# Kernel optimization log

Hardware: AMD Instinct MI355X
Metric: run time of the kernel (lower is better)

The kernel has to match this reference:

```python
import jax, jax.numpy as jnp
import numpy as np

B, N, D = 2, 1024, 64
H, DK, DV = 4, 16, 16
DOUT = 128
STEPS = 3


def _ln(x, eps, w=None, b=None):
    mu = jnp.mean(x, axis=-1, keepdims=True)
    var = jnp.mean((x - mu) ** 2, axis=-1, keepdims=True)
    y = (x - mu) * jax.lax.rsqrt(var + eps)
    if w is not None:
        y = y * w + b
    return y


def setup_inputs() -> dict:
    key = jax.random.key(0)
    ks = jax.random.split(key, 16)
    q_x = jax.random.normal(ks[0], (B, N, D), jnp.float32)
    v_x = jax.random.normal(ks[1], (B, N, D), jnp.float32)
    qa = jax.random.uniform(ks[2], (B, N, N), jnp.float32)
    va = jax.random.uniform(ks[3], (B, N, N), jnp.float32)
    q_adj = qa / jnp.sum(qa, axis=-1, keepdims=True)  # row-normalized adjacency
    v_adj = va / jnp.sum(va, axis=-1, keepdims=True)
    s = 0.05
    w_qs = jax.random.normal(ks[4], (D, H * DK), jnp.float32) * s
    w_ks = jax.random.normal(ks[5], (D, H * DK), jnp.float32) * s
    w_vs = jax.random.normal(ks[6], (D, H * DV), jnp.float32) * s
    w_fc = jax.random.normal(ks[7], (H * DV, D), jnp.float32) * s
    mha_ln_w = jnp.ones((D,), jnp.float32)
    mha_ln_b = jnp.zeros((D,), jnp.float32)
    conv_w = jax.random.normal(ks[8], (D, DOUT), jnp.float32) * s
    conv_b = jnp.zeros((DOUT,), jnp.float32)
    lin_w = jax.random.normal(ks[9], (DOUT, D), jnp.float32) * s
    lin_b = jnp.zeros((D,), jnp.float32)
    norm_w = jnp.ones((D,), jnp.float32)
    norm_b = jnp.zeros((D,), jnp.float32)
    return dict(q_x=q_x, q_adj=q_adj, v_x=v_x, v_adj=v_adj,
                w_qs=w_qs, w_ks=w_ks, w_vs=w_vs, w_fc=w_fc,
                mha_ln_w=mha_ln_w, mha_ln_b=mha_ln_b,
                conv_w=conv_w, conv_b=conv_b, lin_w=lin_w, lin_b=lin_b,
                norm_w=norm_w, norm_b=norm_b)


def reference(q_x, q_adj, v_x, v_adj, w_qs, w_ks, w_vs, w_fc,
              mha_ln_w, mha_ln_b, conv_w, conv_b, lin_w, lin_b,
              norm_w, norm_b):
    b, n, d = q_x.shape
    residual = q_x
    qs, vs = [q_x], [v_x]
    q1 = jnp.einsum('bij,bjd->bid', q_adj, q_x)
    v1 = jnp.einsum('bij,bjd->bid', v_adj, v_x)
    qs.append(q1); vs.append(v1)
    for _ in range(2, STEPS):
        q1 = jnp.einsum('bij,bjd->bid', q_adj, q1)
        v1 = jnp.einsum('bij,bjd->bid', v_adj, v1)
        qs.append(q1); vs.append(v1)
    qc = _ln(jnp.concatenate(qs, axis=1), 1e-5)  # [b, STEPS*n, d]
    vc = _ln(jnp.concatenate(vs, axis=1), 1e-5)
    L = qc.shape[1]
    # multi-head attention (dropout = identity in eval)
    q = (qc @ w_qs).reshape(b, L, H, DK)
    k = (qc @ w_ks).reshape(b, L, H, DK)
    v = (vc @ w_vs).reshape(b, L, H, DV)
    scores = jnp.einsum('bqhd,bkhd->bhqk', q, k) / jnp.asarray(DK ** 0.5, q.dtype)
    attn = jax.nn.softmax(scores, axis=-1)
    o = jnp.einsum('bhqk,bkhd->bqhd', attn, v).reshape(b, L, H * DV)
    o = o @ w_fc + qc
    o = _ln(o, 1e-6, mha_ln_w, mha_ln_b)
    # pool across diffusion steps (faithful to original reshape semantics)
    x = jnp.mean(o.reshape(b, n, -1, STEPS), axis=-1)  # [b, n, d]
    x1 = jax.nn.relu(x @ conv_w + conv_b)
    x = residual + x1 @ lin_w + lin_b
    return _ln(x, 1e-5, norm_w, norm_b)
```

## Files before the change

kernel.cpp:

```cpp
#include <hip/hip_runtime.h>
#include <hip/hip_bf16.h>

#define B_ 2
#define N_ 1024
#define D_ 64
#define L_ 3072
#define H_ 4

typedef __attribute__((ext_vector_type(8))) short s8v;
typedef __attribute__((ext_vector_type(4))) short s4v;
typedef __attribute__((ext_vector_type(4))) float f32x4;

#define EXP2F(x) __builtin_amdgcn_exp2f(x)
#define QSCALE 0.36067376022224085f

__device__ __forceinline__ float wave_sum64(float v) {
#pragma unroll
    for (int off = 32; off > 0; off >>= 1) v += __shfl_xor(v, off, 64);
    return v;
}

__device__ __forceinline__ short f2bf(float f) {
    unsigned u = __float_as_uint(f);
    u += 0x7FFFu + ((u >> 16) & 1u);
    return (short)(u >> 16);
}
__device__ __forceinline__ unsigned cvt_pk_bf16(float a, float b) {
    unsigned r;
    asm("v_cvt_pk_bf16_f32 %0, %1, %2" : "=v"(r) : "v"(a), "v"(b));
    return r;
}
union pk8 { s8v v; unsigned u[4]; };
union pk4 { s4v v; unsigned u[2]; };

__device__ __forceinline__ s8v ldfrag_full(const __hip_bfloat16* p0, const __hip_bfloat16* p1) {
    s4v a = *reinterpret_cast<const s4v*>(p0);
    s4v b = *reinterpret_cast<const s4v*>(p1);
    s8v r;
    r[0] = a[0]; r[1] = a[1]; r[2] = a[2]; r[3] = a[3];
    r[4] = b[0]; r[5] = b[1]; r[6] = b[2]; r[7] = b[3];
    return r;
}
__device__ __forceinline__ s8v wfrag_build(const float* __restrict__ W, int N, int ct, int ks,
                                           int lo, int hi, float scale) {
    s8v r;
    int n = ct * 16 + lo;
    int k0 = ks * 32 + 4 * hi;
#pragma unroll
    for (int j = 0; j < 4; ++j) {
        r[j]     = f2bf(W[(k0 + j) * N + n] * scale);
        r[4 + j] = f2bf(W[(k0 + 16 + j) * N + n] * scale);
    }
    return r;
}

__global__ void xpose(const float* __restrict__ xq, const float* __restrict__ xv,
                      __hip_bfloat16* __restrict__ xtq, __hip_bfloat16* __restrict__ xtv) {
    __shared__ short ts[64][65];
    int m = blockIdx.y;
    int qv = m >> 1, b = m & 1;
    int l0 = blockIdx.x * 64;
    const float* x = (qv ? xv : xq) + (size_t)b * N_ * 64;
    int t = threadIdx.x;
#pragma unroll
    for (int i = 0; i < 4; ++i) {
        int f = t + i * 256;
        int r = f >> 4, c4 = f & 15;
        float4 v = *reinterpret_cast<const float4*>(x + (size_t)(l0 + r) * 64 + c4 * 4);
        ts[c4 * 4 + 0][r] = f2bf(v.x);
        ts[c4 * 4 + 1][r] = f2bf(v.y);
        ts[c4 * 4 + 2][r] = f2bf(v.z);
        ts[c4 * 4 + 3][r] = f2bf(v.w);
    }
    __syncthreads();
    short* xt = reinterpret_cast<short*>(qv ? xtv : xtq) + (size_t)b * 64 * N_;
#pragma unroll
    for (int i = 0; i < 4; ++i) {
        int f = t + i * 256;
        int d = f >> 4, seg = f & 15;
        s4v o;
        o[0] = ts[d][seg * 4 + 0]; o[1] = ts[d][seg * 4 + 1];
        o[2] = ts[d][seg * 4 + 2]; o[3] = ts[d][seg * 4 + 3];
        *reinterpret_cast<s4v*>(xt + (size_t)d * N_ + l0 + seg * 4) = o;
    }
}

__global__ __launch_bounds__(256) void spmm_mfma(
        const float* __restrict__ adj_q, const float* __restrict__ adj_v,
        const __hip_bfloat16* __restrict__ xtq, const __hip_bfloat16* __restrict__ xtv,
        float* __restrict__ oq, float* __restrict__ ov,
        __hip_bfloat16* __restrict__ oqt, __hip_bfloat16* __restrict__ ovt, int writet) {
    const int lane = threadIdx.x & 63;
    const int w = threadIdx.x >> 6;
    const int lo = lane & 15, hi = lane >> 4;
    const int rt = blockIdx.x;
    const int qv = blockIdx.y, b = blockIdx.z;

    const float* adj = (qv ? adj_v : adj_q) + (size_t)b * N_ * N_ + (size_t)(rt * 16 + lo) * N_;
    const __hip_bfloat16* xt = (qv ? xtv : xtq) + ((size_t)b * 64 + w * 16 + lo) * N_;

    f32x4 acc = {0.f, 0.f, 0.f, 0.f};
#pragma unroll 8
    for (int ks = 0; ks < 32; ++ks) {
        int k0 = ks * 32;
        float4 a4 = *reinterpret_cast<const float4*>(adj + k0 + 4 * hi);
        float4 b4 = *reinterpret_cast<const float4*>(adj + k0 + 16 + 4 * hi);
        pk8 af;
        af.u[0] = cvt_pk_bf16(a4.x, a4.y); af.u[1] = cvt_pk_bf16(a4.z, a4.w);
        af.u[2] = cvt_pk_bf16(b4.x, b4.y); af.u[3] = cvt_pk_bf16(b4.z, b4.w);
        s8v xf = ldfrag_full(xt + k0 + 4 * hi, xt + k0 + 16 + 4 * hi);
        acc = __builtin_amdgcn_mfma_f32_16x16x32_bf16(xf, af.v, acc, 0, 0, 0);
    }
    float* o = (qv ? ov : oq) + ((size_t)b * N_ + rt * 16 + lo) * 64 + w * 16 + 4 * hi;
    *reinterpret_cast<f32x4*>(o) = acc;
    if (writet) {
        short* ot = reinterpret_cast<short*>(qv ? ovt : oqt) + (size_t)b * 64 * N_;
#pragma unroll
        for (int j = 0; j < 4; ++j)
            ot[(size_t)(w * 16 + 4 * hi + j) * N_ + rt * 16 + lo] = f2bf(acc[j]);
    }
}

__global__ void concat_ln(const float* __restrict__ qx, const float* __restrict__ q1,
                          const float* __restrict__ q2,
                          const float* __restrict__ vx, const float* __restrict__ v1,
                          const float* __restrict__ v2,
                          float* __restrict__ qc,
                          __hip_bfloat16* __restrict__ qcb, __hip_bfloat16* __restrict__ vcb) {
    int rid  = blockIdx.x * 4 + (threadIdx.x >> 6);
    int lane = threadIdx.x & 63;
    int qvsel = rid >= (B_ * L_);
    int r = qvsel ? rid - B_ * L_ : rid;
    int b = r / L_, l = r % L_;
    int s = l / N_, i = l % N_;
    const float* src;
    if (!qvsel) src = (s == 0) ? qx : (s == 1) ? q1 : q2;
    else        src = (s == 0) ? vx : (s == 1) ? v1 : v2;
    float v = src[((size_t)b * N_ + i) * D_ + lane];
    float mean = wave_sum64(v) * (1.0f / 64.0f);
    float d = v - mean;
    float var = wave_sum64(d * d) * (1.0f / 64.0f);
    float y = d * rsqrtf(var + 1e-5f);
    size_t o = ((size_t)b * L_ + l) * D_ + lane;
    if (!qvsel) {
        qc[o] = y;
        reinterpret_cast<short*>(qcb)[o] = f2bf(y);
    } else {
        reinterpret_cast<short*>(vcb)[o] = f2bf(y);
    }
}

__global__ __launch_bounds__(256) void gemm_qkv(
        const __hip_bfloat16* __restrict__ qcb, const __hip_bfloat16* __restrict__ vcb,
        const float* __restrict__ wq, const float* __restrict__ wk, const float* __restrict__ wv,
        __hip_bfloat16* __restrict__ qpk, __hip_bfloat16* __restrict__ kpk,
        __hip_bfloat16* __restrict__ vpk) {
    const int w = threadIdx.x >> 6;
    const int lane = threadIdx.x & 63;
    const int lo = lane & 15, hi = lane >> 4;
    const int ct0 = w * 3;

    s8v wf[3][2];
#pragma unroll
    for (int c = 0; c < 3; ++c) {
        int ct = ct0 + c;
        const float* W = (ct < 4) ? wq : (ct < 8) ? wk : wv;
        float sc = (ct < 4) ? QSCALE : 1.0f;
        wf[c][0] = wfrag_build(W, 64, ct & 3, 0, lo, hi, sc);
        wf[c][1] = wfrag_build(W, 64, ct & 3, 1, lo, hi, sc);
    }
    const bool needq = (ct0 < 8);
    const bool needv = (ct0 + 2 >= 8);
    const f32x4 zz = {0.f, 0.f, 0.f, 0.f};

#pragma unroll
    for (int rr = 0; rr < 2; ++rr) {
        int rt = blockIdx.x * 2 + rr;
        int rbase = rt * 16;
        int b = rbase / L_;
        int lloc = rbase % L_;
        int t32 = lloc >> 5;
        int half = (lloc >> 4) & 1;
        s8v aq0, aq1, av0, av1;
        if (needq) {
            const __hip_bfloat16* ar = qcb + (size_t)(rbase + lo) * 64;
            aq0 = ldfrag_full(ar + 4 * hi, ar + 16 + 4 * hi);
            aq1 = ldfrag_full(ar + 32 + 4 * hi, ar + 48 + 4 * hi);
        }
        if (needv) {
            const __hip_bfloat16* ar = vcb + (size_t)(rbase + lo) * 64;
            av0 = ldfrag_full(ar + 4 * hi, ar + 16 + 4 * hi);
            av1 = ldfrag_full(ar + 32 + 4 * hi, ar + 48 + 4 * hi);
        }
#pragma unroll
        for (int c = 0; c < 3; ++c) {
            int ct = ct0 + c;
            f32x4 acc = zz;
            if (ct < 8) {
                acc = __builtin_amdgcn_mfma_f32_16x16x32_bf16(wf[c][0], aq0, acc, 0, 0, 0);
                acc = __builtin_amdgcn_mfma_f32_16x16x32_bf16(wf[c][1], aq1, acc, 0, 0, 0);
                int h = ct & 3;
                int bh = b * H_ + h;
                short* dst = reinterpret_cast<short*>((ct < 4) ? qpk : kpk);
                pk4 o;
                o.u[0] = cvt_pk_bf16(acc[0], acc[1]);
                o.u[1] = cvt_pk_bf16(acc[2], acc[3]);
                *reinterpret_cast<s4v*>(dst +
                    (((size_t)bh * 96 + t32) * 64 + lane) * 8 + half * 4) = o.v;
            } else {
                acc = __builtin_amdgcn_mfma_f32_16x16x32_bf16(wf[c][0], av0, acc, 0, 0, 0);
                acc = __builtin_amdgcn_mfma_f32_16x16x32_bf16(wf[c][1], av1, acc, 0, 0, 0);
                int h = ct - 8;
                int bh = b * H_ + h;
                short* vt = reinterpret_cast<short*>(vpk);
                size_t base = ((size_t)bh * 96 + t32) * 64 * 8;
#pragma unroll
                for (int j = 0; j < 4; ++j) {
                    int lanep = (lo >> 2) * 16 + (4 * hi + j);
                    vt[base + (size_t)lanep * 8 + half * 4 + (lo & 3)] = f2bf(acc[j]);
                }
            }
        }
    }
}

__global__ __launch_bounds__(512) void attn_mfma(
        const __hip_bfloat16* __restrict__ qpk, const __hip_bfloat16* __restrict__ kpk,
        const __hip_bfloat16* __restrict__ vpk, __hip_bfloat16* __restrict__ attnob) {
    const int lane = threadIdx.x & 63;
    const int kg = threadIdx.x >> 6;
    const int g = blockIdx.x;
    const int bh = g / 96;
    const int tp = g % 96;
    const int b = bh >> 2, h = bh & 3;
    const int lo = lane & 15, hi = lane >> 4;

    const s8v* kp = reinterpret_cast<const s8v*>(kpk) + ((size_t)bh * 96) * 64 + lane;
    const s8v* vp = reinterpret_cast<const s8v*>(vpk) + ((size_t)bh * 96) * 64 + lane;
    const s8v* qp = reinterpret_cast<const s8v*>(qpk) + ((size_t)bh * 96 + tp) * 64 + lane;

    s8v q8 = *qp;
    s8v qfA = {q8[0], q8[1], q8[2], q8[3], 0, 0, 0, 0};
    s8v qfB = {q8[4], q8[5], q8[6], q8[7], 0, 0, 0, 0};

    f32x4 accA = {0.f, 0.f, 0.f, 0.f}, accB = {0.f, 0.f, 0.f, 0.f};
    float lsA = 0.f, lsB = 0.f;
    const f32x4 zz = {0.f, 0.f, 0.f, 0.f};

    const int t0 = kg * 12;
    s8v kb0 = kp[(size_t)(t0 + 0) * 64];
    s8v vb0 = vp[(size_t)(t0 + 0) * 64];
    s8v kb1 = kp[(size_t)(t0 + 1) * 64];
    s8v vb1 = vp[(size_t)(t0 + 1) * 64];

#pragma unroll
    for (int i = 0; i < 12; ++i) {
        s8v ck, cv;
        if ((i & 1) == 0) { ck = kb0; cv = vb0; }
        else              { ck = kb1; cv = vb1; }
        int pf = (i + 2 < 12) ? t0 + i + 2 : t0;
        if ((i & 1) == 0) { kb0 = kp[(size_t)pf * 64]; vb0 = vp[(size_t)pf * 64]; }
        else              { kb1 = kp[(size_t)pf * 64]; vb1 = vp[(size_t)pf * 64]; }

        s8v kf0 = {ck[0], ck[1], ck[2], ck[3], 0, 0, 0, 0};
        s8v kf1 = {ck[4], ck[5], ck[6], ck[7], 0, 0, 0, 0};

        f32x4 s0A = __builtin_amdgcn_mfma_f32_16x16x32_bf16(kf0, qfA, zz, 0, 0, 0);
        f32x4 s1A = __builtin_amdgcn_mfma_f32_16x16x32_bf16(kf1, qfA, zz, 0, 0, 0);
        f32x4 s0B = __builtin_amdgcn_mfma_f32_16x16x32_bf16(kf0, qfB, zz, 0, 0, 0);
        f32x4 s1B = __builtin_amdgcn_mfma_f32_16x16x32_bf16(kf1, qfB, zz, 0, 0, 0);

        float pA0 = EXP2F(s0A[0]), pA1 = EXP2F(s0A[1]), pA2 = EXP2F(s0A[2]), pA3 = EXP2F(s0A[3]);
        float pA4 = EXP2F(s1A[0]), pA5 = EXP2F(s1A[1]), pA6 = EXP2F(s1A[2]), pA7 = EXP2F(s1A[3]);
        float pB0 = EXP2F(s0B[0]), pB1 = EXP2F(s0B[1]), pB2 = EXP2F(s0B[2]), pB3 = EXP2F(s0B[3]);
        float pB4 = EXP2F(s1B[0]), pB5 = EXP2F(s1B[1]), pB6 = EXP2F(s1B[2]), pB7 = EXP2F(s1B[3]);
        lsA += ((pA0 + pA1) + (pA2 + pA3)) + ((pA4 + pA5) + (pA6 + pA7));
        lsB += ((pB0 + pB1) + (pB2 + pB3)) + ((pB4 + pB5) + (pB6 + pB7));

        pk8 pfA, pfB;
        pfA.u[0] = cvt_pk_bf16(pA0, pA1); pfA.u[1] = cvt_pk_bf16(pA2, pA3);
        pfA.u[2] = cvt_pk_bf16(pA4, pA5); pfA.u[3] = cvt_pk_bf16(pA6, pA7);
        pfB.u[0] = cvt_pk_bf16(pB0, pB1); pfB.u[1] = cvt_pk_bf16(pB2, pB3);
        pfB.u[2] = cvt_pk_bf16(pB4, pB5); pfB.u[3] = cvt_pk_bf16(pB6, pB7);

        accA = __builtin_amdgcn_mfma_f32_16x16x32_bf16(cv, pfA.v, accA, 0, 0, 0);
        accB = __builtin_amdgcn_mfma_f32_16x16x32_bf16(cv, pfB.v, accB, 0, 0, 0);
    }

    lsA += __shfl_xor(lsA, 16, 64); lsA += __shfl_xor(lsA, 32, 64);
    lsB += __shfl_xor(lsB, 16, 64); lsB += __shfl_xor(lsB, 32, 64);

    __shared__ float red[8][2][64][5];
    red[kg][0][lane][0] = accA[0]; red[kg][0][lane][1] = accA[1];
    red[kg][0][lane][2] = accA[2]; red[kg][0][lane][3] = accA[3];
    red[kg][0][lane][4] = lsA;
    red[kg][1][lane][0] = accB[0]; red[kg][1][lane][1] = accB[1];
    red[kg][1][lane][2] = accB[2]; red[kg][1][lane][3] = accB[3];
    red[kg][1][lane][4] = lsB;
    __syncthreads();
    if (kg < 2) {
        int t = kg;
        float a0 = 0.f, a1 = 0.f, a2 = 0.f, a3 = 0.f, lt = 0.f;
#pragma unroll
        for (int g2 = 0; g2 < 8; ++g2) {
            a0 += red[g2][t][lane][0];
            a1 += red[g2][t][lane][1];
            a2 += red[g2][t][lane][2];
            a3 += red[g2][t][lane][3];
            lt += red[g2][t][lane][4];
        }
        float inv = 1.0f / lt;
        pk4 o;
        o.u[0] = cvt_pk_bf16(a0 * inv, a1 * inv);
        o.u[1] = cvt_pk_bf16(a2 * inv, a3 * inv);
        *reinterpret_cast<s4v*>(reinterpret_cast<short*>(attnob) +
            ((size_t)b * L_ + tp * 32 + t * 16 + lo) * 64 + h * 16 + 4 * hi) = o.v;
    }
}

__global__ __launch_bounds__(256) void gemm_fc_ln(
        const __hip_bfloat16* __restrict__ attnob, const float* __restrict__ qc,
        const float* __restrict__ wfc,
        const float* __restrict__ lnw, const float* __restrict__ lnb,
        float* __restrict__ o2) {
    const int rt = blockIdx.x * 4 + (threadIdx.x >> 6);
    const int lane = threadIdx.x & 63;
    const int lo = lane & 15, hi = lane >> 4;
    const f32x4 zz = {0.f, 0.f, 0.f, 0.f};

    s8v wf[4][2];
#pragma unroll
    for (int ct = 0; ct < 4; ++ct) {
        wf[ct][0] = wfrag_build(wfc, 64, ct, 0, lo, hi, 1.0f);
        wf[ct][1] = wfrag_build(wfc, 64, ct, 1, lo, hi, 1.0f);
    }
    const __hip_bfloat16* ar = attnob + (size_t)(rt * 16 + lo) * 64;
    s8v a0 = ldfrag_full(ar + 4 * hi, ar + 16 + 4 * hi);
    s8v a1 = ldfrag_full(ar + 32 + 4 * hi, ar + 48 + 4 * hi);

    f32x4 acc[4];
    const int row = rt * 16 + lo;
#pragma unroll
    for (int ct = 0; ct < 4; ++ct) {
        acc[ct] = zz;
        acc[ct] = __builtin_amdgcn_mfma_f32_16x16x32_bf16(wf[ct][0], a0, acc[ct], 0, 0, 0);
        acc[ct] = __builtin_amdgcn_mfma_f32_16x16x32_bf16(wf[ct][1], a1, acc[ct], 0, 0, 0);
        f32x4 rq = *reinterpret_cast<const f32x4*>(qc + (size_t)row * 64 + ct * 16 + 4 * hi);
        acc[ct][0] += rq[0]; acc[ct][1] += rq[1]; acc[ct][2] += rq[2]; acc[ct][3] += rq[3];
    }
    float s = 0.f;
#pragma unroll
    for (int ct = 0; ct < 4; ++ct) s += (acc[ct][0] + acc[ct][1]) + (acc[ct][2] + acc[ct][3]);
    s += __shfl_xor(s, 16, 64); s += __shfl_xor(s, 32, 64);
    float mean = s * (1.0f / 64.0f);
    float vs = 0.f;
#pragma unroll
    for (int ct = 0; ct < 4; ++ct) {
#pragma unroll
        for (int j = 0; j < 4; ++j) { float d = acc[ct][j] - mean; vs += d * d; }
    }
    vs += __shfl_xor(vs, 16, 64); vs += __shfl_xor(vs, 32, 64);
    float rsq = rsqrtf(vs * (1.0f / 64.0f) + 1e-6f);
#pragma unroll
    for (int ct = 0; ct < 4; ++ct) {
        f32x4 w4 = *reinterpret_cast<const f32x4*>(lnw + ct * 16 + 4 * hi);
        f32x4 b4 = *reinterpret_cast<const f32x4*>(lnb + ct * 16 + 4 * hi);
        f32x4 o;
#pragma unroll
        for (int j = 0; j < 4; ++j) o[j] = (acc[ct][j] - mean) * rsq * w4[j] + b4[j];
        *reinterpret_cast<f32x4*>(o2 + (size_t)row * 64 + ct * 16 + 4 * hi) = o;
    }
}

__global__ void pool_k(const float* __restrict__ o2, __hip_bfloat16* __restrict__ xb) {
    int rid  = blockIdx.x * 4 + (threadIdx.x >> 6);
    int lane = threadIdx.x & 63;
    int b = rid / N_, i = rid % N_;
    const float* ob = o2 + (size_t)b * L_ * 64 + (size_t)192 * i;
    int t = 3 * lane;
    float xv = (ob[t] + ob[t + 1] + ob[t + 2]) * (1.0f / 3.0f);
    reinterpret_cast<short*>(xb)[(size_t)rid * 64 + lane] = f2bf(xv);
}

__global__ __launch_bounds__(256) void gemm_conv(
        const __hip_bfloat16* __restrict__ xb, const float* __restrict__ convw,
        const float* __restrict__ convb, __hip_bfloat16* __restrict__ x1b) {
    const int w = threadIdx.x >> 6;
    const int lane = threadIdx.x & 63;
    const int lo = lane & 15, hi = lane >> 4;
    const int rt = blockIdx.x;
    const f32x4 zz = {0.f, 0.f, 0.f, 0.f};

    s8v wf[2][2];
#pragma unroll
    for (int c = 0; c < 2; ++c) {
        int ct = 2 * w + c;
        wf[c][0] = wfrag_build(convw, 128, ct, 0, lo, hi, 1.0f);
        wf[c][1] = wfrag_build(convw, 128, ct, 1, lo, hi, 1.0f);
    }
    const __hip_bfloat16* ar = xb + (size_t)(rt * 16 + lo) * 64;
    s8v a0 = ldfrag_full(ar + 4 * hi, ar + 16 + 4 * hi);
    s8v a1 = ldfrag_full(ar + 32 + 4 * hi, ar + 48 + 4 * hi);

#pragma unroll
    for (int c = 0; c < 2; ++c) {
        int ct = 2 * w + c;
        f32x4 acc = zz;
        acc = __builtin_amdgcn_mfma_f32_16x16x32_bf16(wf[c][0], a0, acc, 0, 0, 0);
        acc = __builtin_amdgcn_mfma_f32_16x16x32_bf16(wf[c][1], a1, acc, 0, 0, 0);
        f32x4 bia = *reinterpret_cast<const f32x4*>(convb + ct * 16 + 4 * hi);
        pk4 o;
        o.u[0] = cvt_pk_bf16(fmaxf(acc[0] + bia[0], 0.f), fmaxf(acc[1] + bia[1], 0.f));
        o.u[1] = cvt_pk_bf16(fmaxf(acc[2] + bia[2], 0.f), fmaxf(acc[3] + bia[3], 0.f));
        *reinterpret_cast<s4v*>(reinterpret_cast<short*>(x1b) +
            (size_t)(rt * 16 + lo) * 128 + ct * 16 + 4 * hi) = o.v;
    }
}

__global__ __launch_bounds__(256) void gemm_lin_ln(
        const __hip_bfloat16* __restrict__ x1b, const float* __restrict__ qx,
        const float* __restrict__ linw, const float* __restrict__ linb,
        const float* __restrict__ nw, const float* __restrict__ nb,
        float* __restrict__ out) {
    const int rt = blockIdx.x * 4 + (threadIdx.x >> 6);
    const int lane = threadIdx.x & 63;
    const int lo = lane & 15, hi = lane >> 4;
    const f32x4 zz = {0.f, 0.f, 0.f, 0.f};

    s8v wf[4][4];
#pragma unroll
    for (int ct = 0; ct < 4; ++ct)
#pragma unroll
        for (int ks = 0; ks < 4; ++ks)
            wf[ct][ks] = wfrag_build(linw, 64, ct, ks, lo, hi, 1.0f);

    const __hip_bfloat16* ar = x1b + (size_t)(rt * 16 + lo) * 128;
    s8v af[4];
#pragma unroll
    for (int ks = 0; ks < 4; ++ks)
        af[ks] = ldfrag_full(ar + ks * 32 + 4 * hi, ar + ks * 32 + 16 + 4 * hi);

    f32x4 acc[4];
    const int row = rt * 16 + lo;
#pragma unroll
    for (int ct = 0; ct < 4; ++ct) {
        acc[ct] = zz;
#pragma unroll
        for (int ks = 0; ks < 4; ++ks)
            acc[ct] = __builtin_amdgcn_mfma_f32_16x16x32_bf16(wf[ct][ks], af[ks], acc[ct], 0, 0, 0);
        f32x4 bia = *reinterpret_cast<const f32x4*>(linb + ct * 16 + 4 * hi);
        f32x4 rq  = *reinterpret_cast<const f32x4*>(qx + (size_t)row * 64 + ct * 16 + 4 * hi);
#pragma unroll
        for (int j = 0; j < 4; ++j) acc[ct][j] += bia[j] + rq[j];
    }
    float s = 0.f;
#pragma unroll
    for (int ct = 0; ct < 4; ++ct) s += (acc[ct][0] + acc[ct][1]) + (acc[ct][2] + acc[ct][3]);
    s += __shfl_xor(s, 16, 64); s += __shfl_xor(s, 32, 64);
    float mean = s * (1.0f / 64.0f);
    float vs = 0.f;
#pragma unroll
    for (int ct = 0; ct < 4; ++ct) {
#pragma unroll
        for (int j = 0; j < 4; ++j) { float d = acc[ct][j] - mean; vs += d * d; }
    }
    vs += __shfl_xor(vs, 16, 64); vs += __shfl_xor(vs, 32, 64);
    float rsq = rsqrtf(vs * (1.0f / 64.0f) + 1e-5f);
#pragma unroll
    for (int ct = 0; ct < 4; ++ct) {
        f32x4 w4 = *reinterpret_cast<const f32x4*>(nw + ct * 16 + 4 * hi);
        f32x4 b4 = *reinterpret_cast<const f32x4*>(nb + ct * 16 + 4 * hi);
        f32x4 o;
#pragma unroll
        for (int j = 0; j < 4; ++j) o[j] = (acc[ct][j] - mean) * rsq * w4[j] + b4[j];
        *reinterpret_cast<f32x4*>(out + (size_t)row * 64 + ct * 16 + 4 * hi) = o;
    }
}

extern "C" void kernel_launch(void* const* d_in, const int* in_sizes, int n_in,
                              void* d_out, int out_size, void* d_ws, size_t ws_size,
                              hipStream_t stream) {
    const float* q_x      = (const float*)d_in[0];
    const float* q_adj    = (const float*)d_in[1];
    const float* v_x      = (const float*)d_in[2];
    const float* v_adj    = (const float*)d_in[3];
    const float* w_qs     = (const float*)d_in[4];
    const float* w_ks     = (const float*)d_in[5];
    const float* w_vs     = (const float*)d_in[6];
    const float* w_fc     = (const float*)d_in[7];
    const float* mha_ln_w = (const float*)d_in[8];
    const float* mha_ln_b = (const float*)d_in[9];
    const float* conv_w   = (const float*)d_in[10];
    const float* conv_b   = (const float*)d_in[11];
    const float* lin_w    = (const float*)d_in[12];
    const float* lin_b    = (const float*)d_in[13];
    const float* norm_w   = (const float*)d_in[14];
    const float* norm_b   = (const float*)d_in[15];

    float* ws = (float*)d_ws;
    float* q1    = ws;
    float* v1    = q1 + 131072;
    float* q2    = v1 + 131072;
    float* v2    = q2 + 131072;
    float* qc    = v2 + 131072;
    float* o2    = qc + 393216;
    __hip_bfloat16* qcb    = (__hip_bfloat16*)(o2 + 393216);
    __hip_bfloat16* vcb    = qcb + 393216;
    __hip_bfloat16* qpk    = vcb + 393216;
    __hip_bfloat16* kpk    = qpk + 393216;
    __hip_bfloat16* vpk    = kpk + 393216;
    __hip_bfloat16* attnob = vpk + 393216;
    __hip_bfloat16* xtq    = attnob + 393216;
    __hip_bfloat16* xtv    = xtq + 131072;
    __hip_bfloat16* q1t    = xtv + 131072;
    __hip_bfloat16* v1t    = q1t + 131072;
    __hip_bfloat16* xb     = v1t + 131072;
    __hip_bfloat16* x1b    = xb + 131072;
    float* out   = (float*)d_out;

    xpose<<<dim3(16, 4), 256, 0, stream>>>(q_x, v_x, xtq, xtv);
    spmm_mfma<<<dim3(64, 2, 2), 256, 0, stream>>>(q_adj, v_adj, xtq, xtv,
                                                  q1, v1, q1t, v1t, 1);
    spmm_mfma<<<dim3(64, 2, 2), 256, 0, stream>>>(q_adj, v_adj, q1t, v1t,
                                                  q2, v2, nullptr, nullptr, 0);
    concat_ln<<<3072, 256, 0, stream>>>(q_x, q1, q2, v_x, v1, v2, qc, qcb, vcb);
    gemm_qkv<<<192, 256, 0, stream>>>(qcb, vcb, w_qs, w_ks, w_vs, qpk, kpk, vpk);
    attn_mfma<<<768, 512, 0, stream>>>(qpk, kpk, vpk, attnob);
    gemm_fc_ln<<<96, 256, 0, stream>>>(attnob, qc, w_fc, mha_ln_w, mha_ln_b, o2);
    pool_k<<<512, 256, 0, stream>>>(o2, xb);
    gemm_conv<<<128, 256, 0, stream>>>(xb, conv_w, conv_b, x1b);
    gemm_lin_ln<<<32, 256, 0, stream>>>(x1b, q_x, lin_w, lin_b, norm_w, norm_b, out);
}
```

Before: 163.6 us.

## Fuse concat-LayerNorm into QKV GEMM and fuse pool/conv/lin tail kernels

The concat+LayerNorm step is folded into the QKV projection kernel: each block normalizes its 32 rows of q and v into shared-memory bf16 tiles and feeds the MFMAs from LDS, so the qcb/vcb intermediates are no longer written or read. The pooling, conv GEMM, ReLU and lin GEMM+LayerNorm are merged into one kernel that keeps its intermediates in shared memory. Together this removes three kernel launches and several global round trips. In exchange, the tail LayerNorm now goes through an extra LDS stage with block barriers, and the lin GEMM runs on 128 smaller blocks instead of 32.

New measurement: 153.0 us. 1.07x faster.

```diff
diff --git a/kernel.cpp b/kernel.cpp
--- a/kernel.cpp
+++ b/kernel.cpp
@@ -14,12 +14,6 @@
 #define EXP2F(x) __builtin_amdgcn_exp2f(x)
 #define QSCALE 0.36067376022224085f
 
-__device__ __forceinline__ float wave_sum64(float v) {
-#pragma unroll
-    for (int off = 32; off > 0; off >>= 1) v += __shfl_xor(v, off, 64);
-    return v;
-}
-
 __device__ __forceinline__ short f2bf(float f) {
     unsigned u = __float_as_uint(f);
     u += 0x7FFFu + ((u >> 16) & 1u);
@@ -34,6 +28,14 @@
 union pk4 { s4v v; unsigned u[2]; };
 
 __device__ __forceinline__ s8v ldfrag_full(const __hip_bfloat16* p0, const __hip_bfloat16* p1) {
+    s4v a = *reinterpret_cast<const s4v*>(p0);
+    s4v b = *reinterpret_cast<const s4v*>(p1);
+    s8v r;
+    r[0] = a[0]; r[1] = a[1]; r[2] = a[2]; r[3] = a[3];
+    r[4] = b[0]; r[5] = b[1]; r[6] = b[2]; r[7] = b[3];
+    return r;
+}
+__device__ __forceinline__ s8v ldsfrag(const short* p0, const short* p1) {
     s4v a = *reinterpret_cast<const s4v*>(p0);
     s4v b = *reinterpret_cast<const s4v*>(p1);
     s8v r;
@@ -121,45 +123,22 @@
     }
 }
 
-__global__ void concat_ln(const float* __restrict__ qx, const float* __restrict__ q1,
-                          const float* __restrict__ q2,
-                          const float* __restrict__ vx, const float* __restrict__ v1,
-                          const float* __restrict__ v2,
-                          float* __restrict__ qc,
-                          __hip_bfloat16* __restrict__ qcb, __hip_bfloat16* __restrict__ vcb) {
-    int rid  = blockIdx.x * 4 + (threadIdx.x >> 6);
-    int lane = threadIdx.x & 63;
-    int qvsel = rid >= (B_ * L_);
-    int r = qvsel ? rid - B_ * L_ : rid;
-    int b = r / L_, l = r % L_;
-    int s = l / N_, i = l % N_;
-    const float* src;
-    if (!qvsel) src = (s == 0) ? qx : (s == 1) ? q1 : q2;
-    else        src = (s == 0) ? vx : (s == 1) ? v1 : v2;
-    float v = src[((size_t)b * N_ + i) * D_ + lane];
-    float mean = wave_sum64(v) * (1.0f / 64.0f);
-    float d = v - mean;
-    float var = wave_sum64(d * d) * (1.0f / 64.0f);
-    float y = d * rsqrtf(var + 1e-5f);
-    size_t o = ((size_t)b * L_ + l) * D_ + lane;
-    if (!qvsel) {
-        qc[o] = y;
-        reinterpret_cast<short*>(qcb)[o] = f2bf(y);
-    } else {
-        reinterpret_cast<short*>(vcb)[o] = f2bf(y);
-    }
-}
-
-__global__ __launch_bounds__(256) void gemm_qkv(
-        const __hip_bfloat16* __restrict__ qcb, const __hip_bfloat16* __restrict__ vcb,
+__global__ __launch_bounds__(256) void gemm_qkv_ln(
+        const float* __restrict__ qx, const float* __restrict__ q1, const float* __restrict__ q2,
+        const float* __restrict__ vx, const float* __restrict__ v1, const float* __restrict__ v2,
         const float* __restrict__ wq, const float* __restrict__ wk, const float* __restrict__ wv,
+        float* __restrict__ qc,
         __hip_bfloat16* __restrict__ qpk, __hip_bfloat16* __restrict__ kpk,
         __hip_bfloat16* __restrict__ vpk) {
     const int w = threadIdx.x >> 6;
     const int lane = threadIdx.x & 63;
     const int lo = lane & 15, hi = lane >> 4;
+    const int rbase = blockIdx.x * 32;
+
+    __shared__ short qs[32][72];
+    __shared__ short vs[32][72];
+
     const int ct0 = w * 3;
-
     s8v wf[3][2];
 #pragma unroll
     for (int c = 0; c < 3; ++c) {
@@ -169,29 +148,79 @@
         wf[c][0] = wfrag_build(W, 64, ct & 3, 0, lo, hi, sc);
         wf[c][1] = wfrag_build(W, 64, ct & 3, 1, lo, hi, sc);
     }
-    const bool needq = (ct0 < 8);
-    const bool needv = (ct0 + 2 >= 8);
+
+    {
+        const int isv = (w >= 2);
+        const int r = (w & 1) * 16 + (lane >> 2);
+        const int cg = lane & 3;
+        const int grow = rbase + r;
+        const int b = grow / L_;
+        const int l = grow % L_;
+        const int s = l / N_, i = l % N_;
+        const float* src;
+        if (!isv) src = (s == 0) ? qx : (s == 1) ? q1 : q2;
+        else      src = (s == 0) ? vx : (s == 1) ? v1 : v2;
+        const float* p = src + ((size_t)b * N_ + i) * 64 + cg * 16;
+        f32x4 x0 = *reinterpret_cast<const f32x4*>(p);
+        f32x4 x1 = *reinterpret_cast<const f32x4*>(p + 4);
+        f32x4 x2 = *reinterpret_cast<const f32x4*>(p + 8);
+        f32x4 x3 = *reinterpret_cast<const f32x4*>(p + 12);
+        float sum = (x0[0]+x0[1]+x0[2]+x0[3]) + (x1[0]+x1[1]+x1[2]+x1[3])
+                  + (x2[0]+x2[1]+x2[2]+x2[3]) + (x3[0]+x3[1]+x3[2]+x3[3]);
+        sum += __shfl_xor(sum, 1, 64);
+        sum += __shfl_xor(sum, 2, 64);
+        float mean = sum * (1.0f / 64.0f);
+        float vsum = 0.f;
+        float y[16];
+#pragma unroll
+        for (int j = 0; j < 4; ++j) { float d = x0[j]-mean; y[j]    = d; vsum += d*d; }
+#pragma unroll
+        for (int j = 0; j < 4; ++j) { float d = x1[j]-mean; y[4+j]  = d; vsum += d*d; }
+#pragma unroll
+        for (int j = 0; j < 4; ++j) { float d = x2[j]-mean; y[8+j]  = d; vsum += d*d; }
+#pragma unroll
+        for (int j = 0; j < 4; ++j) { float d = x3[j]-mean; y[12+j] = d; vsum += d*d; }
+        vsum += __shfl_xor(vsum, 1, 64);
+        vsum += __shfl_xor(vsum, 2, 64);
+        float rsq = rsqrtf(vsum * (1.0f / 64.0f) + 1e-5f);
+#pragma unroll
+        for (int j = 0; j < 16; ++j) y[j] *= rsq;
+        pk8 pa, pb;
+        pa.u[0] = cvt_pk_bf16(y[0], y[1]);  pa.u[1] = cvt_pk_bf16(y[2], y[3]);
+        pa.u[2] = cvt_pk_bf16(y[4], y[5]);  pa.u[3] = cvt_pk_bf16(y[6], y[7]);
+        pb.u[0] = cvt_pk_bf16(y[8], y[9]);  pb.u[1] = cvt_pk_bf16(y[10], y[11]);
+        pb.u[2] = cvt_pk_bf16(y[12], y[13]); pb.u[3] = cvt_pk_bf16(y[14], y[15]);
+        short* dst = (isv ? &vs[r][0] : &qs[r][0]) + cg * 16;
+        *reinterpret_cast<s8v*>(dst)     = pa.v;
+        *reinterpret_cast<s8v*>(dst + 8) = pb.v;
+        if (!isv) {
+            float* qcd = qc + (size_t)grow * 64 + cg * 16;
+#pragma unroll
+            for (int j = 0; j < 4; ++j) qcd[j]      = y[j];
+#pragma unroll
+            for (int j = 0; j < 4; ++j) qcd[4 + j]  = y[4 + j];
+#pragma unroll
+            for (int j = 0; j < 4; ++j) qcd[8 + j]  = y[8 + j];
+#pragma unroll
+            for (int j = 0; j < 4; ++j) qcd[12 + j] = y[12 + j];
+        }
+    }
+    __syncthreads();
+
     const f32x4 zz = {0.f, 0.f, 0.f, 0.f};
-
 #pragma unroll
     for (int rr = 0; rr < 2; ++rr) {
-        int rt = blockIdx.x * 2 + rr;
-        int rbase = rt * 16;
-        int b = rbase / L_;
-        int lloc = rbase % L_;
+        int rbase16 = rbase + rr * 16;
+        int b = rbase16 / L_;
+        int lloc = rbase16 % L_;
         int t32 = lloc >> 5;
         int half = (lloc >> 4) & 1;
-        s8v aq0, aq1, av0, av1;
-        if (needq) {
-            const __hip_bfloat16* ar = qcb + (size_t)(rbase + lo) * 64;
-            aq0 = ldfrag_full(ar + 4 * hi, ar + 16 + 4 * hi);
-            aq1 = ldfrag_full(ar + 32 + 4 * hi, ar + 48 + 4 * hi);
-        }
-        if (needv) {
-            const __hip_bfloat16* ar = vcb + (size_t)(rbase + lo) * 64;
-            av0 = ldfrag_full(ar + 4 * hi, ar + 16 + 4 * hi);
-            av1 = ldfrag_full(ar + 32 + 4 * hi, ar + 48 + 4 * hi);
-        }
+        const short* arq = &qs[rr * 16 + lo][0];
+        const short* arv = &vs[rr * 16 + lo][0];
+        s8v aq0 = ldsfrag(arq + 4 * hi, arq + 16 + 4 * hi);
+        s8v aq1 = ldsfrag(arq + 32 + 4 * hi, arq + 48 + 4 * hi);
+        s8v av0 = ldsfrag(arv + 4 * hi, arv + 16 + 4 * hi);
+        s8v av1 = ldsfrag(arv + 32 + 4 * hi, arv + 48 + 4 * hi);
 #pragma unroll
         for (int c = 0; c < 3; ++c) {
             int ct = ct0 + c;
@@ -372,108 +401,107 @@
     }
 }
 
-__global__ void pool_k(const float* __restrict__ o2, __hip_bfloat16* __restrict__ xb) {
-    int rid  = blockIdx.x * 4 + (threadIdx.x >> 6);
-    int lane = threadIdx.x & 63;
-    int b = rid / N_, i = rid % N_;
-    const float* ob = o2 + (size_t)b * L_ * 64 + (size_t)192 * i;
-    int t = 3 * lane;
-    float xv = (ob[t] + ob[t + 1] + ob[t + 2]) * (1.0f / 3.0f);
-    reinterpret_cast<short*>(xb)[(size_t)rid * 64 + lane] = f2bf(xv);
-}
-
-__global__ __launch_bounds__(256) void gemm_conv(
-        const __hip_bfloat16* __restrict__ xb, const float* __restrict__ convw,
-        const float* __restrict__ convb, __hip_bfloat16* __restrict__ x1b) {
+__global__ __launch_bounds__(256) void tail_fused(
+        const float* __restrict__ o2, const float* __restrict__ convw,
+        const float* __restrict__ convb, const float* __restrict__ linw,
+        const float* __restrict__ linb, const float* __restrict__ qx,
+        const float* __restrict__ nw, const float* __restrict__ nb,
+        float* __restrict__ out) {
     const int w = threadIdx.x >> 6;
     const int lane = threadIdx.x & 63;
     const int lo = lane & 15, hi = lane >> 4;
     const int rt = blockIdx.x;
-    const f32x4 zz = {0.f, 0.f, 0.f, 0.f};
-
-    s8v wf[2][2];
+
+    __shared__ short xs[16][68];
+    __shared__ short x1s[16][136];
+    __shared__ float accs[16][68];
+
+    s8v cwf[2][2];
 #pragma unroll
     for (int c = 0; c < 2; ++c) {
         int ct = 2 * w + c;
-        wf[c][0] = wfrag_build(convw, 128, ct, 0, lo, hi, 1.0f);
-        wf[c][1] = wfrag_build(convw, 128, ct, 1, lo, hi, 1.0f);
-    }
-    const __hip_bfloat16* ar = xb + (size_t)(rt * 16 + lo) * 64;
-    s8v a0 = ldfrag_full(ar + 4 * hi, ar + 16 + 4 * hi);
-    s8v a1 = ldfrag_full(ar + 32 + 4 * hi, ar + 48 + 4 * hi);
-
-#pragma unroll
-    for (int c = 0; c < 2; ++c) {
-        int ct = 2 * w + c;
-        f32x4 acc = zz;
-        acc = __builtin_amdgcn_mfma_f32_16x16x32_bf16(wf[c][0], a0, acc, 0, 0, 0);
-        acc = __builtin_amdgcn_mfma_f32_16x16x32_bf16(wf[c][1], a1, acc, 0, 0, 0);
-        f32x4 bia = *reinterpret_cast<const f32x4*>(convb + ct * 16 + 4 * hi);
-        pk4 o;
-        o.u[0] = cvt_pk_bf16(fmaxf(acc[0] + bia[0], 0.f), fmaxf(acc[1] + bia[1], 0.f));
-        o.u[1] = cvt_pk_bf16(fmaxf(acc[2] + bia[2], 0.f), fmaxf(acc[3] + bia[3], 0.f));
-        *reinterpret_cast<s4v*>(reinterpret_cast<short*>(x1b) +
-            (size_t)(rt * 16 + lo) * 128 + ct * 16 + 4 * hi) = o.v;
-    }
-}
-
-__global__ __launch_bounds__(256) void gemm_lin_ln(
-        const __hip_bfloat16* __restrict__ x1b, const float* __restrict__ qx,
-        const float* __restrict__ linw, const float* __restrict__ linb,
-        const float* __restrict__ nw, const float* __restrict__ nb,
-        float* __restrict__ out) {
-    const int rt = blockIdx.x * 4 + (threadIdx.x >> 6);
-    const int lane = threadIdx.x & 63;
-    const int lo = lane & 15, hi = lane >> 4;
-    const f32x4 zz = {0.f, 0.f, 0.f, 0.f};
-
-    s8v wf[4][4];
-#pragma unroll
-    for (int ct = 0; ct < 4; ++ct)
+        cwf[c][0] = wfrag_build(convw, 128, ct, 0, lo, hi, 1.0f);
+        cwf[c][1] = wfrag_build(convw, 128, ct, 1, lo, hi, 1.0f);
+    }
+    s8v lwf[4];
+#pragma unroll
+    for (int ks = 0; ks < 4; ++ks)
+        lwf[ks] = wfrag_build(linw, 64, w, ks, lo, hi, 1.0f);
+
+#pragma unroll
+    for (int i = 0; i < 4; ++i) {
+        int f = threadIdx.x + i * 256;
+        int r = f >> 6, c = f & 63;
+        int rid = rt * 16 + r;
+        int b = rid >> 10, ii = rid & 1023;
+        const float* ob = o2 + (size_t)b * (L_ * 64) + 192 * ii + 3 * c;
+        xs[r][c] = f2bf((ob[0] + ob[1] + ob[2]) * (1.0f / 3.0f));
+    }
+    __syncthreads();
+
+    {
+        const short* ar = &xs[lo][0];
+        s8v a0 = ldsfrag(ar + 4 * hi, ar + 16 + 4 * hi);
+        s8v a1 = ldsfrag(ar + 32 + 4 * hi, ar + 48 + 4 * hi);
+        const f32x4 zz = {0.f, 0.f, 0.f, 0.f};
+#pragma unroll
+        for (int c = 0; c < 2; ++c) {
+            int ct = 2 * w + c;
+            f32x4 acc = zz;
+            acc = __builtin_amdgcn_mfma_f32_16x16x32_bf16(cwf[c][0], a0, acc, 0, 0, 0);
+            acc = __builtin_amdgcn_mfma_f32_16x16x32_bf16(cwf[c][1], a1, acc, 0, 0, 0);
+            f32x4 bia = *reinterpret_cast<const f32x4*>(convb + ct * 16 + 4 * hi);
+            pk4 o;
+            o.u[0] = cvt_pk_bf16(fmaxf(acc[0] + bia[0], 0.f), fmaxf(acc[1] + bia[1], 0.f));
+            o.u[1] = cvt_pk_bf16(fmaxf(acc[2] + bia[2], 0.f), fmaxf(acc[3] + bia[3], 0.f));
+            *reinterpret_cast<s4v*>(&x1s[lo][ct * 16 + 4 * hi]) = o.v;
+        }
+    }
+    __syncthreads();
+
+    {
+        const short* br = &x1s[lo][0];
+        s8v af[4];
 #pragma unroll
         for (int ks = 0; ks < 4; ++ks)
-            wf[ct][ks] = wfrag_build(linw, 64, ct, ks, lo, hi, 1.0f);
-
-    const __hip_bfloat16* ar = x1b + (size_t)(rt * 16 + lo) * 128;
-    s8v af[4];
-#pragma unroll
-    for (int ks = 0; ks < 4; ++ks)
-        af[ks] = ldfrag_full(ar + ks * 32 + 4 * hi, ar + ks * 32 + 16 + 4 * hi);
-
-    f32x4 acc[4];
-    const int row = rt * 16 + lo;
-#pragma unroll
-    for (int ct = 0; ct < 4; ++ct) {
-        acc[ct] = zz;
+            af[ks] = ldsfrag(br + ks * 32 + 4 * hi, br + ks * 32 + 16 + 4 * hi);
+        f32x4 acc = {0.f, 0.f, 0.f, 0.f};
 #pragma unroll
         for (int ks = 0; ks < 4; ++ks)
-            acc[ct] = __builtin_amdgcn_mfma_f32_16x16x32_bf16(wf[ct][ks], af[ks], acc[ct], 0, 0, 0);
-        f32x4 bia = *reinterpret_cast<const f32x4*>(linb + ct * 16 + 4 * hi);
-        f32x4 rq  = *reinterpret_cast<const f32x4*>(qx + (size_t)row * 64 + ct * 16 + 4 * hi);
-#pragma unroll
-        for (int j = 0; j < 4; ++j) acc[ct][j] += bia[j] + rq[j];
-    }
-    float s = 0.f;
-#pragma unroll
-    for (int ct = 0; ct < 4; ++ct) s += (acc[ct][0] + acc[ct][1]) + (acc[ct][2] + acc[ct][3]);
-    s += __shfl_xor(s, 16, 64); s += __shfl_xor(s, 32, 64);
-    float mean = s * (1.0f / 64.0f);
-    float vs = 0.f;
-#pragma unroll
-    for (int ct = 0; ct < 4; ++ct) {
-#pragma unroll
-        for (int j = 0; j < 4; ++j) { float d = acc[ct][j] - mean; vs += d * d; }
-    }
-    vs += __shfl_xor(vs, 16, 64); vs += __shfl_xor(vs, 32, 64);
-    float rsq = rsqrtf(vs * (1.0f / 64.0f) + 1e-5f);
-#pragma unroll
-    for (int ct = 0; ct < 4; ++ct) {
-        f32x4 w4 = *reinterpret_cast<const f32x4*>(nw + ct * 16 + 4 * hi);
-        f32x4 b4 = *reinterpret_cast<const f32x4*>(nb + ct * 16 + 4 * hi);
+            acc = __builtin_amdgcn_mfma_f32_16x16x32_bf16(lwf[ks], af[ks], acc, 0, 0, 0);
+        int rid = rt * 16 + lo;
+        f32x4 bia = *reinterpret_cast<const f32x4*>(linb + w * 16 + 4 * hi);
+        f32x4 rq  = *reinterpret_cast<const f32x4*>(qx + (size_t)rid * 64 + w * 16 + 4 * hi);
+#pragma unroll
+        for (int j = 0; j < 4; ++j) accs[lo][w * 16 + 4 * hi + j] = acc[j] + bia[j] + rq[j];
+    }
+    __syncthreads();
+
+    {
+        int r = 4 * w + hi;
+        f32x4 v4 = *reinterpret_cast<const f32x4*>(&accs[r][lo * 4]);
+        float sum = (v4[0] + v4[1]) + (v4[2] + v4[3]);
+        sum += __shfl_xor(sum, 1, 64);
+        sum += __shfl_xor(sum, 2, 64);
+        sum += __shfl_xor(sum, 4, 64);
+        sum += __shfl_xor(sum, 8, 64);
+        float mean = sum * (1.0f / 64.0f);
+        f32x4 d4;
+        float vsum = 0.f;
+#pragma unroll
+        for (int j = 0; j < 4; ++j) { d4[j] = v4[j] - mean; vsum += d4[j] * d4[j]; }
+        vsum += __shfl_xor(vsum, 1, 64);
+        vsum += __shfl_xor(vsum, 2, 64);
+        vsum += __shfl_xor(vsum, 4, 64);
+        vsum += __shfl_xor(vsum, 8, 64);
+        float rsq = rsqrtf(vsum * (1.0f / 64.0f) + 1e-5f);
+        f32x4 w4 = *reinterpret_cast<const f32x4*>(nw + lo * 4);
+        f32x4 b4 = *reinterpret_cast<const f32x4*>(nb + lo * 4);
         f32x4 o;
 #pragma unroll
-        for (int j = 0; j < 4; ++j) o[j] = (acc[ct][j] - mean) * rsq * w4[j] + b4[j];
-        *reinterpret_cast<f32x4*>(out + (size_t)row * 64 + ct * 16 + 4 * hi) = o;
+        for (int j = 0; j < 4; ++j) o[j] = d4[j] * rsq * w4[j] + b4[j];
+        int rid = rt * 16 + r;
+        *reinterpret_cast<f32x4*>(out + (size_t)rid * 64 + lo * 4) = o;
     }
 }
 
@@ -504,9 +532,7 @@
     float* v2    = q2 + 131072;
     float* qc    = v2 + 131072;
     float* o2    = qc + 393216;
-    __hip_bfloat16* qcb    = (__hip_bfloat16*)(o2 + 393216);
-    __hip_bfloat16* vcb    = qcb + 393216;
-    __hip_bfloat16* qpk    = vcb + 393216;
+    __hip_bfloat16* qpk    = (__hip_bfloat16*)(o2 + 393216);
     __hip_bfloat16* kpk    = qpk + 393216;
     __hip_bfloat16* vpk    = kpk + 393216;
     __hip_bfloat16* attnob = vpk + 393216;
@@ -514,8 +540,6 @@
     __hip_bfloat16* xtv    = xtq + 131072;
     __hip_bfloat16* q1t    = xtv + 131072;
     __hip_bfloat16* v1t    = q1t + 131072;
-    __hip_bfloat16* xb     = v1t + 131072;
-    __hip_bfloat16* x1b    = xb + 131072;
     float* out   = (float*)d_out;
 
     xpose<<<dim3(16, 4), 256, 0, stream>>>(q_x, v_x, xtq, xtv);
@@ -523,11 +547,10 @@
                                                   q1, v1, q1t, v1t, 1);
     spmm_mfma<<<dim3(64, 2, 2), 256, 0, stream>>>(q_adj, v_adj, q1t, v1t,
                                                   q2, v2, nullptr, nullptr, 0);
-    concat_ln<<<3072, 256, 0, stream>>>(q_x, q1, q2, v_x, v1, v2, qc, qcb, vcb);
-    gemm_qkv<<<192, 256, 0, stream>>>(qcb, vcb, w_qs, w_ks, w_vs, qpk, kpk, vpk);
+    gemm_qkv_ln<<<192, 256, 0, stream>>>(q_x, q1, q2, v_x, v1, v2,
+                                         w_qs, w_ks, w_vs, qc, qpk, kpk, vpk);
     attn_mfma<<<768, 512, 0, stream>>>(qpk, kpk, vpk, attnob);
     gemm_fc_ln<<<96, 256, 0, stream>>>(attnob, qc, w_fc, mha_ln_w, mha_ln_b, o2);
-    pool_k<<<512, 256, 0, stream>>>(o2, xb);
-    gemm_conv<<<128, 256, 0, stream>>>(xb, conv_w, conv_b, x1b);
-    gemm_lin_ln<<<32, 256, 0, stream>>>(x1b, q_x, lin_w, lin_b, norm_w, norm_b, out);
-}
+    tail_fused<<<128, 256, 0, stream>>>(o2, conv_w, conv_b, lin_w, lin_b,
+                                        q_x, norm_w, norm_b, out);
+}
```
